# Performance work log

Hardware: AMD Instinct MI355X
Metric: run time of the kernel (lower is better)

Reference implementation:

```python
import jax, jax.numpy as jnp
import numpy as np
from jax import lax

# Fixed Sobel kernels, OIHW layout: [2 out, 1 in, 3, 3]
_GX = np.array([[1, 0, -1], [2, 0, -2], [1, 0, -1]], dtype=np.float32)
_GY = np.array([[1, 2, 1], [0, 0, 0], [-1, -2, -1]], dtype=np.float32)
SOBEL_K = jnp.asarray(np.stack([_GX, _GY], 0)[:, None])  # [2,1,3,3]


def setup_inputs() -> dict:
    key = jax.random.key(0)
    x = jax.random.normal(key, (16, 1, 1024, 1024), dtype=jnp.float32)
    return {"x": x}


def reference(x):
    # Sobel conv, padding=1 (SAME): y [B,2,H,W]
    y = lax.conv_general_dilated(
        x, SOBEL_K, window_strides=(1, 1), padding=((1, 1), (1, 1)),
        dimension_numbers=("NCHW", "OIHW", "NCHW"))
    # sb_x: cross-correlation with [1,-1] along W -> s[:, :-1] - s[:, 1:], then drop last row
    s0 = jnp.sign(y[:, 0:1])                       # [B,1,H,W]
    y0 = (s0[..., :-1] - s0[..., 1:])[..., :-1, :]  # [B,1,H-1,W-1]
    # sb_y: cross-correlation with [1,-1]^T along H -> s[:-1] - s[1:], then drop last col
    s1 = jnp.sign(y[:, 1:2])                       # [B,1,H,W]
    y1 = (s1[..., :-1, :] - s1[..., 1:, :])[..., :-1]  # [B,1,H-1,W-1]
    return (y, y0, y1)
```

## Files before the change

### kernel.cpp

```cpp
#include <hip/hip_runtime.h>


__device__ __forceinline__ void load_row(const float* __restrict__ xb, int r, int t,
                                         double* __restrict__ o ) {
    int rc = min(max(r, 0), 1023);
    float m = ((unsigned)r < 1024u) ? 1.0f : 0.0f;
    const float4* __restrict__ rp = (const float4*)(xb + (rc << 10));
    float4 L = rp[(t > 0) ? (t - 1) : 0];
    float4 C = rp[t];
    float4 R = rp[(t < 255) ? (t + 1) : 255];
    float lw = (t > 0)   ? L.w : 0.0f;
    float r0 = (t < 255) ? R.x : 0.0f;
    float r1 = (t < 255) ? R.y : 0.0f;
    o[0] = (double)(lw  * m);
    o[1] = (double)(C.x * m);
    o[2] = (double)(C.y * m);
    o[3] = (double)(C.z * m);
    o[4] = (double)(C.w * m);
    o[5] = (double)(r0  * m);
    o[6] = (double)(r1  * m);
}

__device__ __forceinline__ float fsign(double v) {
    return (v > 0.0) ? 1.0f : ((v < 0.0) ? -1.0f : 0.0f);
}

__global__ __launch_bounds__(256) void sobel_sign_kernel(const float* __restrict__ x,
                                                         float* __restrict__ out) {
    const int t  = threadIdx.x;
    const int b  = blockIdx.x >> 7;
    const int hg = blockIdx.x & 127;
    const int h0 = hg << 3;
    const int w0 = t << 2;

    const float* __restrict__ xb = x + ((size_t)b << 20);
    float* __restrict__ yb = out + ((size_t)b << 21);
    const size_t NP    = (size_t)1023 * 1023;
    const size_t Y0    = 33554432u + (size_t)b * NP;
    const size_t Y1    = 50298896u + (size_t)b * NP;

    double r[3][7];
    load_row(xb, h0 - 1, t, r[0]);
    load_row(xb, h0,     t, r[1]);

    float psgy[4];

    #pragma unroll
    for (int it = 0; it < 8; ++it) {
        const int h = h0 + it;
        double* A0 = r[it % 3];
        double* A1 = r[(it + 1) % 3];
        double* A2 = r[(it + 2) % 3];
        load_row(xb, h + 1, t, A2);

        double tc[7], d[6];
        #pragma unroll
        for (int c = 0; c < 7; ++c) tc[c] = A0[c] + 2.0 * A1[c] + A2[c];
        #pragma unroll
        for (int c = 0; c < 6; ++c) d[c] = A0[c] - A2[c];

        double gx[5];
        #pragma unroll
        for (int j = 0; j < 5; ++j) gx[j] = tc[j] - tc[j + 2];
        double gy[4];
        #pragma unroll
        for (int j = 0; j < 4; ++j) gy[j] = d[j] + 2.0 * d[j + 1] + d[j + 2];

        size_t yo = ((size_t)h << 10) + (size_t)w0;
        *(float4*)(yb + yo) =
            make_float4((float)gx[0], (float)gx[1], (float)gx[2], (float)gx[3]);
        *(float4*)(yb + yo + (1u << 20)) =
            make_float4((float)gy[0], (float)gy[1], (float)gy[2], (float)gy[3]);

        float sgx[5], sgy[4];
        #pragma unroll
        for (int j = 0; j < 5; ++j) sgx[j] = fsign(gx[j]);
        #pragma unroll
        for (int j = 0; j < 4; ++j) sgy[j] = fsign(gy[j]);

        if (h < 1023) {
            size_t p = Y0 + (size_t)h * 1023u + (size_t)w0;
            #pragma unroll
            for (int j = 0; j < 4; ++j)
                if (w0 + j < 1023) out[p + j] = sgx[j] - sgx[j + 1];
        }
        if (it > 0) {
            size_t p = Y1 + (size_t)(h - 1) * 1023u + (size_t)w0;
            #pragma unroll
            for (int j = 0; j < 4; ++j)
                if (w0 + j < 1023) out[p + j] = psgy[j] - sgy[j];
        }
        #pragma unroll
        for (int j = 0; j < 4; ++j) psgy[j] = sgy[j];
    }

    const int hl = h0 + 7;
    if (hl < 1023) {
        double* B0 = r[8 % 3];
        double bn[7];
        load_row(xb, hl + 2, t, bn);
        double d2[6];
        #pragma unroll
        for (int c = 0; c < 6; ++c) d2[c] = B0[c] - bn[c];
        size_t p = Y1 + (size_t)hl * 1023u + (size_t)w0;
        #pragma unroll
        for (int j = 0; j < 4; ++j) {
            double gyn = d2[j] + 2.0 * d2[j + 1] + d2[j + 2];
            if (w0 + j < 1023) out[p + j] = psgy[j] - fsign(gyn);
        }
    }
}

extern "C" void kernel_launch(void* const* d_in, const int* in_sizes, int n_in,
                              void* d_out, int out_size, void* d_ws, size_t ws_size,
                              hipStream_t stream) {
    const float* x = (const float*)d_in[0];
    float* out = (float*)d_out;
    dim3 grid(16 * 128), block(256);
    sobel_sign_kernel<<<grid, block, 0, stream>>>(x, out);
}
```

Measured before the change: 354.7 us.

## Stage sign-difference outputs through LDS for coalesced stores and prefetch next row

```diff
diff --git a/kernel.cpp b/kernel.cpp
--- a/kernel.cpp
+++ b/kernel.cpp
@@ -1,24 +1,25 @@
 #include <hip/hip_runtime.h>
 
 
-__device__ __forceinline__ void load_row(const float* __restrict__ xb, int r, int t,
-                                         double* __restrict__ o ) {
-    int rc = min(max(r, 0), 1023);
-    float m = ((unsigned)r < 1024u) ? 1.0f : 0.0f;
-    const float4* __restrict__ rp = (const float4*)(xb + (rc << 10));
-    float4 L = rp[(t > 0) ? (t - 1) : 0];
-    float4 C = rp[t];
-    float4 R = rp[(t < 255) ? (t + 1) : 255];
-    float lw = (t > 0)   ? L.w : 0.0f;
-    float r0 = (t < 255) ? R.x : 0.0f;
-    float r1 = (t < 255) ? R.y : 0.0f;
-    o[0] = (double)(lw  * m);
-    o[1] = (double)(C.x * m);
-    o[2] = (double)(C.y * m);
-    o[3] = (double)(C.z * m);
-    o[4] = (double)(C.w * m);
-    o[5] = (double)(r0  * m);
-    o[6] = (double)(r1  * m);
+__device__ __forceinline__ void load_raw(const float* __restrict__ xb, int r, int t,
+                                         float4& L, float4& C, float4& R) {
+    if ((unsigned)r < 1024u) {
+        const float4* __restrict__ rp = (const float4*)(xb + (r << 10));
+        L = rp[(t > 0) ? (t - 1) : 0];
+        C = rp[t];
+        R = rp[(t < 255) ? (t + 1) : 255];
+    } else {
+        L = C = R = make_float4(0.f, 0.f, 0.f, 0.f);
+    }
+}
+
+__device__ __forceinline__ void cvt_row(float4 L, float4 C, float4 R, int t,
+                                        double* __restrict__ o ) {
+    float lw = (t > 0)   ? L.w : 0.f;
+    float r0 = (t < 255) ? R.x : 0.f;
+    float r1 = (t < 255) ? R.y : 0.f;
+    o[0] = (double)lw;  o[1] = (double)C.x; o[2] = (double)C.y; o[3] = (double)C.z;
+    o[4] = (double)C.w; o[5] = (double)r0;  o[6] = (double)r1;
 }
 
 __device__ __forceinline__ float fsign(double v) {
@@ -35,13 +36,18 @@
 
     const float* __restrict__ xb = x + ((size_t)b << 20);
     float* __restrict__ yb = out + ((size_t)b << 21);
-    const size_t NP    = (size_t)1023 * 1023;
-    const size_t Y0    = 33554432u + (size_t)b * NP;
-    const size_t Y1    = 50298896u + (size_t)b * NP;
+    const size_t NP = (size_t)1023 * 1023;
+    float* __restrict__ Y0 = out + 33554432u + (size_t)b * NP;
+    float* __restrict__ Y1 = out + 50298896u + (size_t)b * NP;
+
+    __shared__ float s0[1024];
+    __shared__ float s1[1024];
 
     double r[3][7];
-    load_row(xb, h0 - 1, t, r[0]);
-    load_row(xb, h0,     t, r[1]);
+    float4 L, C, R;
+    load_raw(xb, h0 - 1, t, L, C, R); cvt_row(L, C, R, t, r[0]);
+    load_raw(xb, h0,     t, L, C, R); cvt_row(L, C, R, t, r[1]);
+    load_raw(xb, h0 + 1, t, L, C, R);
 
     float psgy[4];
 
@@ -51,7 +57,8 @@
         double* A0 = r[it % 3];
         double* A1 = r[(it + 1) % 3];
         double* A2 = r[(it + 2) % 3];
-        load_row(xb, h + 1, t, A2);
+        cvt_row(L, C, R, t, A2);
+        load_raw(xb, h + 2, t, L, C, R);
 
         double tc[7], d[6];
         #pragma unroll
@@ -59,10 +66,9 @@
         #pragma unroll
         for (int c = 0; c < 6; ++c) d[c] = A0[c] - A2[c];
 
-        double gx[5];
+        double gx[5], gy[4];
         #pragma unroll
         for (int j = 0; j < 5; ++j) gx[j] = tc[j] - tc[j + 2];
-        double gy[4];
         #pragma unroll
         for (int j = 0; j < 4; ++j) gy[j] = d[j] + 2.0 * d[j + 1] + d[j + 2];
 
@@ -78,35 +84,48 @@
         #pragma unroll
         for (int j = 0; j < 4; ++j) sgy[j] = fsign(gy[j]);
 
-        if (h < 1023) {
-            size_t p = Y0 + (size_t)h * 1023u + (size_t)w0;
-            #pragma unroll
-            for (int j = 0; j < 4; ++j)
-                if (w0 + j < 1023) out[p + j] = sgx[j] - sgx[j + 1];
+        __syncthreads();
+        #pragma unroll
+        for (int j = 0; j < 4; ++j) {
+            s0[w0 + j] = sgx[j] - sgx[j + 1];
+            s1[w0 + j] = (it > 0) ? (psgy[j] - sgy[j]) : 0.f;
         }
-        if (it > 0) {
-            size_t p = Y1 + (size_t)(h - 1) * 1023u + (size_t)w0;
-            #pragma unroll
-            for (int j = 0; j < 4; ++j)
-                if (w0 + j < 1023) out[p + j] = psgy[j] - sgy[j];
+        __syncthreads();
+        #pragma unroll
+        for (int k = 0; k < 4; ++k) {
+            int c = t + (k << 8);
+            bool cok = c < 1023;
+            if (h < 1023 && cok) Y0[(size_t)h * 1023u + c] = s0[c];
+            if (it > 0 && cok)   Y1[(size_t)(h - 1) * 1023u + c] = s1[c];
         }
         #pragma unroll
         for (int j = 0; j < 4; ++j) psgy[j] = sgy[j];
     }
 
-    const int hl = h0 + 7;
-    if (hl < 1023) {
-        double* B0 = r[8 % 3];
+    {
+        const int hl = h0 + 7;
         double bn[7];
-        load_row(xb, hl + 2, t, bn);
-        double d2[6];
-        #pragma unroll
-        for (int c = 0; c < 6; ++c) d2[c] = B0[c] - bn[c];
-        size_t p = Y1 + (size_t)hl * 1023u + (size_t)w0;
+        cvt_row(L, C, R, t, bn);
+        double* B0 = r[2];
+        float y1v[4];
         #pragma unroll
         for (int j = 0; j < 4; ++j) {
-            double gyn = d2[j] + 2.0 * d2[j + 1] + d2[j + 2];
-            if (w0 + j < 1023) out[p + j] = psgy[j] - fsign(gyn);
+            double d0 = B0[j]     - bn[j];
+            double d1 = B0[j + 1] - bn[j + 1];
+            double d2 = B0[j + 2] - bn[j + 2];
+            double gyn = d0 + 2.0 * d1 + d2;
+            y1v[j] = psgy[j] - fsign(gyn);
+        }
+        __syncthreads();
+        #pragma unroll
+        for (int j = 0; j < 4; ++j) s1[w0 + j] = y1v[j];
+        __syncthreads();
+        if (hl < 1023) {
+            #pragma unroll
+            for (int k = 0; k < 4; ++k) {
+                int c = t + (k << 8);
+                if (c < 1023) Y1[(size_t)hl * 1023u + c] = s1[c];
+            }
         }
     }
 }
```

Result: faster. 318.6 us (-10.2%).
